# Performance work log

Hardware: AMD Instinct MI355X
Metric: run time of the kernel (lower is better)

## Reference

```python
import jax, jax.numpy as jnp
import numpy as np

B, V, D, R = 2, 4096, 192, 16
E, H = 2 * D, 8
DH = E // H
K, TK = 16, 8


def _ln(x, g, b):
    m = x.mean(-1, keepdims=True)
    v = ((x - m) ** 2).mean(-1, keepdims=True)
    return (x - m) * jax.lax.rsqrt(v + 1e-5) * g + b


def _coords():
    # voxel centers in [-1,1]^3, (V,3)
    r = (jnp.arange(R, dtype=jnp.float32) + 0.5) / R * 2.0 - 1.0
    return jnp.stack(jnp.meshgrid(r, r, r, indexing='ij'), -1).reshape(-1, 3)


def setup_inputs() -> dict:
    key = jax.random.key(0)
    ks = jax.random.split(key, 10)
    s = 0.02
    return {
        'voxel_tokens': jax.random.normal(ks[0], (B, V, D), jnp.float32),
        'non_empty_mask': jax.random.randint(ks[1], (B, V), 0, 2).astype(bool),
        'We': jax.random.normal(ks[2], (D, E)) * s, 'be': jnp.zeros((E,)),
        'g1': jnp.ones((E,)), 'bt1': jnp.zeros((E,)),
        'Wqkv': jax.random.normal(ks[3], (E, 3 * E)) * s, 'bqkv': jnp.zeros((3 * E,)),
        'Wo': jax.random.normal(ks[4], (E, E)) * s, 'bo': jnp.zeros((E,)),
        'Wc': jax.random.normal(ks[5], (E, D)) * s, 'bc': jnp.zeros((D,)),
        'g2': jnp.ones((E,)), 'bt2': jnp.zeros((E,)),
        'W1': jax.random.normal(ks[6], (E, 2 * E)) * s, 'b1': jnp.zeros((2 * E,)),
        'W2': jax.random.normal(ks[7], (2 * E, E)) * s, 'b2': jnp.zeros((E,)),
    }


def reference(voxel_tokens, non_empty_mask, We, be, g1, bt1, Wqkv, bqkv, Wo, bo,
              Wc, bc, g2, bt2, W1, b1, W2, b2):
    fmask = non_empty_mask.astype(voxel_tokens.dtype)  # (B,V)
    shortcut = voxel_tokens
    x = voxel_tokens @ We + be                          # expand: (B,V,E)
    x = _ln(x, g1, bt1)
    # --- sparse dynamic voxel attention ---
    c = _coords()
    d2 = jnp.sum((c[:, None, :] - c[None, :, :]) ** 2, -1)  # (V,V)
    big = jnp.asarray(1e9, x.dtype)
    dmask = d2[None] + (1.0 - fmask)[:, None, :] * big      # empty keys pushed away
    _, knn = jax.lax.top_k(-dmask, K)                        # (B,V,K) nearest non-empty
    qkv = x @ Wqkv + bqkv
    q, k, v = jnp.split(qkv, 3, axis=-1)                     # (B,V,E) each
    bidx = jnp.arange(B)[:, None, None]
    kn = k[bidx, knn].reshape(B, V, K, H, DH)                # gathered neighbor keys
    vn = v[bidx, knn].reshape(B, V, K, H, DH)
    qh = q.reshape(B, V, H, DH)
    scores = jnp.einsum('bvhd,bvkhd->bvhk', qh, kn) / jnp.sqrt(jnp.asarray(DH, x.dtype))
    nvalid = fmask[bidx, knn]                                # (B,V,K)
    scores = jnp.where(nvalid[:, :, None, :] > 0, scores, -big)
    sel, sidx = jax.lax.top_k(scores, TK)                    # top_k_select by score
    attn = jax.nn.softmax(sel, axis=-1)                      # (B,V,H,TK)
    vt = vn.transpose(0, 1, 3, 2, 4)                         # (B,V,H,K,DH)
    vsel = jnp.take_along_axis(vt, sidx[..., None], axis=3)  # (B,V,H,TK,DH)
    o = jnp.einsum('bvhk,bvhkd->bvhd', attn, vsel).reshape(B, V, E)
    o = o @ Wo + bo
    # masked scatter: empty voxels -> zeros (reconstruct_dense_masked_scatter_2)
    x = o * fmask[..., None]
    x = x @ Wc + bc                                          # contract
    x = x * 0.5 + shortcut                                   # DropPath(0) -> identity
    x2 = x @ We + be
    x2 = _ln(x2, g2, bt2)
    x2 = jax.nn.gelu(x2 @ W1 + b1) @ W2 + b2                 # FeedForward(E, 2E)
    x2 = x2 @ Wc + bc
    return x2 * 0.5 + x
```

## Files before the change

kernel.cpp:

```cpp
#include <hip/hip_runtime.h>
#include <stdint.h>


using u16 = unsigned short;
using u32 = unsigned int;
using u64 = unsigned long long;

typedef short short8 __attribute__((ext_vector_type(8)));
typedef float f32x4 __attribute__((ext_vector_type(4)));

#define DEV static __device__ __forceinline__

constexpr int cV = 4096, cD = 192;
constexpr int cE = 384;
constexpr int cKN = 16, cTK = 8;
constexpr int cM = 2 * cV;
constexpr int c3E = 1152;

DEV float bf2f(u16 v) { return __uint_as_float(((u32)v) << 16); }
DEV float bflo(u32 v) { return __uint_as_float(v << 16); }
DEV float bfhi(u32 v) { return __uint_as_float(v & 0xFFFF0000u); }
DEV u16 f2bf(float f) {
  u32 u = __float_as_uint(f);
  u = (u + 0x7FFFu + ((u >> 16) & 1u)) >> 16;
  return (u16)u;
}
DEV int mget(const void* mp, int flag, int i) {
  if (flag == 0) return ((const int*)mp)[i] != 0;
  if (flag == 1) return ((const float*)mp)[i] != 0.0f;
  if (flag == 2) return ((const u16*)mp)[i] != 0;
  return ((const unsigned char*)mp)[i] != 0;
}
DEV float gelu_tanh(float x) {
  float t = tanhf(0.7978845608028654f * (x + 0.044715f * x * x * x));
  return 0.5f * x * (1.0f + t);
}
DEV u32 f2ord(float f) {
  u32 u = __float_as_uint(f);
  return (u & 0x80000000u) ? ~u : (u | 0x80000000u);
}
DEV float ord2f(u32 o) {
  u32 bits = (o & 0x80000000u) ? (o & 0x7FFFFFFFu) : ~o;
  return __uint_as_float(bits);
}
DEV int bf_plausible(u32 h) {
  if (h == 0u || h == 0x8000u) return 1;
  u32 e = (h >> 7) & 0xFFu;
  return (e >= 100u && e <= 140u) ? 1 : 0;
}

using as1p = const unsigned int __attribute__((address_space(1)))*;
using as3p = unsigned int __attribute__((address_space(3)))*;
DEV void gload16(const void* g, void* l) {
  __builtin_amdgcn_global_load_lds((as1p)g, (as3p)l, 16, 0, 0);
}
DEV f32x4 mfma16x16x32_bf16(short8 a, short8 b, f32x4 c) {
  asm volatile("v_mfma_f32_16x16x32_bf16 %0, %1, %2, %0" : "+v"(c) : "v"(a), "v"(b));
  return c;
}
DEV int swz(int row, int byteoff) { return byteoff ^ ((row & 7) << 4); }
DEV int ldswz(int r, int c) { return r * 64 + (c ^ ((r & 7) * 8)); }

#define SBPIN() __builtin_amdgcn_sched_barrier(0)
#define VMW(N) do { \
  __builtin_amdgcn_sched_barrier(0); \
  asm volatile("s_waitcnt vmcnt(" #N ")" ::: "memory"); \
  __builtin_amdgcn_sched_barrier(0); \
} while (0)

template <int T, typename AF>
DEV void stage_1x8(const u16* __restrict__ wbase, int Kst, u16* bpriv,
                   int l15, int l4, int sr, int scs,
                   f32x4 (&acc)[2][3], AF&& aread) {
  #pragma unroll
  for (int i = 0; i < 6; ++i)
    gload16(wbase + (size_t)(i * 8 + sr) * Kst + scs, (char*)bpriv + i * 1024);
  SBPIN();
  #pragma unroll
  for (int t = 0; t < T; ++t) {
    if (t + 1 < T) {
      #pragma unroll
      for (int i = 0; i < 6; ++i)
        gload16(wbase + (size_t)(i * 8 + sr) * Kst + (t + 1) * 64 + scs,
                (char*)bpriv + ((t + 1) & 1) * 6144 + i * 1024);
      VMW(6);
    } else {
      VMW(0);
    }
    const u16* bb = bpriv + (t & 1) * 3072;
    #pragma unroll
    for (int ks = 0; ks < 2; ++ks) {
      short8 a0 = aread(0, t, ks);
      short8 a1 = aread(1, t, ks);
      #pragma unroll
      for (int n = 0; n < 3; ++n) {
        short8 b = *(const short8*)&bb[ldswz(n * 16 + l15, ks * 32 + l4 * 8)];
        acc[0][n] = mfma16x16x32_bf16(a0, b, acc[0][n]);
        acc[1][n] = mfma16x16x32_bf16(a1, b, acc[1][n]);
      }
    }
    SBPIN();
  }
}

template <int T, typename AF>
DEV void stage_2x4(const u16* __restrict__ wbase, int Kst, u16* bpriv,
                   int l15, int l4, int sr, int scs,
                   f32x4 (&acc)[3], AF&& aread) {
  #pragma unroll
  for (int i = 0; i < 6; ++i)
    gload16(wbase + (size_t)(i * 8 + sr) * Kst + scs, (char*)bpriv + i * 1024);
  SBPIN();
  #pragma unroll
  for (int t = 0; t < T; ++t) {
    if (t + 1 < T) {
      #pragma unroll
      for (int i = 0; i < 6; ++i)
        gload16(wbase + (size_t)(i * 8 + sr) * Kst + (t + 1) * 64 + scs,
                (char*)bpriv + ((t + 1) & 1) * 6144 + i * 1024);
      VMW(6);
    } else {
      VMW(0);
    }
    const u16* bb = bpriv + (t & 1) * 3072;
    #pragma unroll
    for (int ks = 0; ks < 2; ++ks) {
      short8 a = aread(t, ks);
      #pragma unroll
      for (int n = 0; n < 3; ++n) {
        short8 b = *(const short8*)&bb[ldswz(n * 16 + l15, ks * 32 + l4 * 8)];
        acc[n] = mfma16x16x32_bf16(a, b, acc[n]);
      }
    }
    SBPIN();
  }
}

__global__ void detect_all_kernel(const u32* __restrict__ tok,
                                  const u32* __restrict__ m,
                                  int* __restrict__ flag) {
  __shared__ int cnt, sa, sb, sc;
  if (threadIdx.x == 0) { cnt = 0; sa = 0; sb = 0; sc = 0; }
  __syncthreads();
  int c = 0;
  for (int i = threadIdx.x; i < 4096; i += 256) {
    u32 d = tok[i];
    c += bf_plausible(d & 0xFFFFu) & bf_plausible(d >> 16);
  }
  atomicAdd(&cnt, c);
  int a = 0, b = 0, cc = 0;
  for (int i = threadIdx.x; i < 2048; i += 256) {
    u32 d = m[i];
    if (!(d == 0u || d == 1u)) a = 1;
    if (!(d == 0u || d == 0x3F800000u)) b = 1;
    if (!(d == 0u || d == 0x00003F80u || d == 0x3F800000u || d == 0x3F803F80u)) cc = 1;
  }
  if (a) atomicOr(&sa, 1);
  if (b) atomicOr(&sb, 1);
  if (cc) atomicOr(&sc, 1);
  __syncthreads();
  if (threadIdx.x == 0) {
    flag[1] = (cnt > 3400) ? 1 : 0;
    flag[0] = (sa == 0) ? 0 : ((sb == 0) ? 1 : ((sc == 0) ? 2 : 3));
  }
}

struct PrepArgs {
  const void* csrc[11]; u16* cdst[11]; int cn[11];
  const void* tsrc[6]; u16* tdst[6]; int tK[6]; int tN[6];
  const void* mask; u64* bm;
};
__global__ __launch_bounds__(256) void prep_kernel(PrepArgs a, const int* __restrict__ flag) {
  const int job = blockIdx.y;
  const int dt = flag[1];
  if (job < 11) {
    const int n = a.cn[job];
    u16* d = a.cdst[job];
    if (dt) {
      const u16* s = (const u16*)a.csrc[job];
      for (int i = blockIdx.x * 256 + threadIdx.x; i < n; i += gridDim.x * 256) d[i] = s[i];
    } else {
      const float* s = (const float*)a.csrc[job];
      for (int i = blockIdx.x * 256 + threadIdx.x; i < n; i += gridDim.x * 256) d[i] = f2bf(s[i]);
    }
  } else if (job < 17) {
    const int t = job - 11;
    const int K = a.tK[t], N = a.tN[t];
    const int total = K * N;
    u16* d = a.tdst[t];
    for (int i = blockIdx.x * 256 + threadIdx.x; i < total; i += gridDim.x * 256) {
      int n = i / K, k = i - n * K;
      u16 vv;
      if (dt) vv = ((const u16*)a.tsrc[t])[(size_t)k * N + n];
      else vv = f2bf(((const float*)a.tsrc[t])[(size_t)k * N + n]);
      d[i] = vv;
    }
  } else {
    const int gw = (blockIdx.x * 256 + threadIdx.x) >> 6;
    const int lane = threadIdx.x & 63;
    if (gw < 128) {
      const int fl = flag[0];
      u64 bal = __ballot(mget(a.mask, fl, gw * 64 + lane) != 0);
      if (lane == 0) a.bm[gw] = bal;
    }
  }
}

__global__ __launch_bounds__(256) void knn_kernel(const u64* __restrict__ bitmask,
                                                  int* __restrict__ knn_out) {
  const int tid = threadIdx.x;
  const int wid = tid >> 6, lane = tid & 63;
  const int q0 = blockIdx.x * 4;
  const int b = q0 >> 12;
  const int q = q0 + wid;
  const int v = q & 4095;
  __shared__ u64 smask[64];
  __shared__ int hist4[4][64];
  __shared__ int listT[4][64];
  __shared__ int out16s[4][16];
  __shared__ int meta[4][3];
  __shared__ int cntA[4], cntT[4];
  if (tid < 64) smask[tid] = bitmask[b * 64 + tid];
  for (int i = tid; i < 4 * 64; i += 256) ((int*)hist4)[i] = 0;
  if (lane == 0) { cntA[wid] = 0; cntT[wid] = 0; }
  __syncthreads();
  const int iv = v >> 8, jv = (v >> 4) & 15, kv = v & 15;
  #pragma unroll
  for (int t = 0; t < 12; ++t) {
    int o = t * 64 + lane;
    if (o < 729) {
      int oi = o / 81, rm = o - oi * 81;
      int oj = rm / 9, ok = rm - oj * 9;
      int i = iv + oi - 4, j = jv + oj - 4, k = kv + ok - 4;
      if (((i | j | k) & ~15) == 0) {
        int u = (i << 8) | (j << 4) | k;
        if ((smask[u >> 6] >> (u & 63)) & 1ull) {
          int di = oi - 4, dj = oj - 4, dk = ok - 4;
          atomicAdd(&hist4[wid][di * di + dj * dj + dk * dk], 1);
        }
      }
    }
  }
  __syncthreads();
  if (lane == 0) {
    int cum = 0, T = -1, below = 0;
    for (int d = 0; d <= 48; ++d) {
      int h = hist4[wid][d];
      if (h > 0 && cum + h >= cKN) { T = d; below = cum; break; }
      cum += h;
    }
    if (T > 24) T = -1;
    meta[wid][0] = T; meta[wid][1] = below; meta[wid][2] = (T < 0) ? 1 : 0;
  }
  __syncthreads();
  const int T = meta[wid][0], below = meta[wid][1], fb = meta[wid][2];
  #pragma unroll
  for (int t = 0; t < 12; ++t) {
    int o = t * 64 + lane;
    if (o < 729) {
      int oi = o / 81, rm = o - oi * 81;
      int oj = rm / 9, ok = rm - oj * 9;
      int i = iv + oi - 4, j = jv + oj - 4, k = kv + ok - 4;
      if (((i | j | k) & ~15) == 0) {
        int u = (i << 8) | (j << 4) | k;
        if ((smask[u >> 6] >> (u & 63)) & 1ull) {
          int di = oi - 4, dj = oj - 4, dk = ok - 4;
          int d2 = di * di + dj * dj + dk * dk;
          if (d2 < T) { int p = atomicAdd(&cntA[wid], 1); out16s[wid][p] = u; }
          else if (d2 == T) { int p = atomicAdd(&cntT[wid], 1); if (p < 64) listT[wid][p] = u; }
        }
      }
    }
  }
  __syncthreads();
  if (!fb) {
    if (lane == 0) {
      int need = cKN - below;
      int nT = cntT[wid] < 64 ? cntT[wid] : 64;
      for (int r = 0; r < need; ++r) {
        int bi = 0, bu = 0x7FFFFFFF;
        for (int i2 = 0; i2 < nT; ++i2) { int x = listT[wid][i2]; if (x < bu) { bu = x; bi = i2; } }
        out16s[wid][below + r] = bu;
        listT[wid][bi] = 0x7FFFFFFF;
      }
    }
  } else {
    u64 rem = smask[lane];
    const int myi = lane >> 2;
    const int di2 = (iv - myi) * (iv - myi);
    for (int r = 0; r < cKN; ++r) {
      u64 tmp = rem;
      u32 best = 0xFFFFFFFFu;
      while (tmp) {
        int bp = __builtin_ctzll(tmp);
        tmp &= tmp - 1;
        int u = (lane << 6) | bp;
        int dj = jv - ((u >> 4) & 15), dk = kv - (u & 15);
        u32 key = (u32)(((di2 + dj * dj + dk * dk) << 12) | u);
        if (key < best) best = key;
      }
      u32 pk = (best == 0xFFFFFFFFu) ? 0xFFFFFFFFu : ((best << 6) | (u32)lane);
      #pragma unroll
      for (int off = 1; off < 64; off <<= 1) {
        u32 o2 = __shfl_xor(pk, off);
        if (o2 < pk) pk = o2;
      }
      int u = (int)((pk >> 6) & 4095u);
      int wl = (int)(pk & 63u);
      if (lane == wl) rem &= ~(1ull << (u & 63));
      if (lane == 0) out16s[wid][r] = u;
    }
  }
  __syncthreads();
  if (lane < cKN) knn_out[q * cKN + lane] = out16s[wid][lane];
}

__global__ __launch_bounds__(512) void fused_ln_qkv(
    const u16* __restrict__ tokc, const u16* __restrict__ WeT,
    const u16* __restrict__ be, const u16* __restrict__ g1, const u16* __restrict__ bt1,
    const u16* __restrict__ WqkvT, const u16* __restrict__ bqkv,
    u16* __restrict__ QB) {
  __shared__ alignas(16) u16 Afull[3 * 2048];
  __shared__ alignas(16) u16 Bst[8][2][3072];
  __shared__ alignas(16) char X1[32 * 768];
  __shared__ float st[32][8][2];
  const int tid = threadIdx.x;
  const int lane = tid & 63, wn = tid >> 6;
  const int l15 = lane & 15, l4 = lane >> 4;
  const int sr = lane >> 3;
  const int scs = (((lane & 7) ^ sr) << 3);
  const int row0 = blockIdx.x * 32;
  u16* bpriv = &Bst[wn][0][0];

  for (int g = wn; g < 12; g += 8)
    gload16(tokc + (size_t)(row0 + (g & 3) * 8 + sr) * 192 + (g >> 2) * 64 + scs,
            (char*)Afull + g * 1024);
  SBPIN();
  __syncthreads();

  f32x4 acc[2][3];
  #pragma unroll
  for (int m = 0; m < 2; ++m)
    #pragma unroll
    for (int n = 0; n < 3; ++n) acc[m][n] = f32x4{0.f, 0.f, 0.f, 0.f};
  stage_1x8<3>(WeT + (size_t)(wn * 48) * 192, 192, bpriv, l15, l4, sr, scs, acc,
               [&](int m, int t, int ks) {
                 return *(const short8*)&Afull[t * 2048 + ldswz(m * 16 + l15, ks * 32 + l4 * 8)];
               });
  float s[2][4], sq[2][4];
  #pragma unroll
  for (int m = 0; m < 2; ++m)
    #pragma unroll
    for (int j = 0; j < 4; ++j) { s[m][j] = 0.f; sq[m][j] = 0.f; }
  #pragma unroll
  for (int n = 0; n < 3; ++n) {
    const float bi = bf2f(be[wn * 48 + n * 16 + l15]);
    #pragma unroll
    for (int m = 0; m < 2; ++m)
      #pragma unroll
      for (int j = 0; j < 4; ++j) {
        acc[m][n][j] += bi;
        s[m][j] += acc[m][n][j]; sq[m][j] += acc[m][n][j] * acc[m][n][j];
      }
  }
  #pragma unroll
  for (int off = 1; off < 16; off <<= 1)
    #pragma unroll
    for (int m = 0; m < 2; ++m)
      #pragma unroll
      for (int j = 0; j < 4; ++j) { s[m][j] += __shfl_xor(s[m][j], off); sq[m][j] += __shfl_xor(sq[m][j], off); }
  if (l15 == 0) {
    #pragma unroll
    for (int m = 0; m < 2; ++m)
      #pragma unroll
      for (int j = 0; j < 4; ++j) {
        const int rl = m * 16 + l4 * 4 + j;
        st[rl][wn][0] = s[m][j]; st[rl][wn][1] = sq[m][j];
      }
  }
  __syncthreads();
  #pragma unroll
  for (int m = 0; m < 2; ++m)
    #pragma unroll
    for (int j = 0; j < 4; ++j) {
      const int rl = m * 16 + l4 * 4 + j;
      float ts = 0.f, tq = 0.f;
      #pragma unroll
      for (int wv = 0; wv < 8; ++wv) { ts += st[rl][wv][0]; tq += st[rl][wv][1]; }
      const float mean = ts * (1.0f / 384.0f);
      const float var = tq * (1.0f / 384.0f) - mean * mean;
      const float rstd = rsqrtf(var + 1e-5f);
      #pragma unroll
      for (int n = 0; n < 3; ++n) {
        const int col = wn * 48 + n * 16 + l15;
        const float v = (acc[m][n][j] - mean) * rstd * bf2f(g1[col]) + bf2f(bt1[col]);
        *(u16*)(X1 + swz(rl, rl * 768 + col * 2)) = f2bf(v);
      }
    }
  __syncthreads();

  for (int chunk = 0; chunk < 3; ++chunk) {
    f32x4 a2[2][3];
    #pragma unroll
    for (int m = 0; m < 2; ++m)
      #pragma unroll
      for (int n = 0; n < 3; ++n) a2[m][n] = f32x4{0.f, 0.f, 0.f, 0.f};
    stage_1x8<6>(WqkvT + (size_t)(chunk * 384 + wn * 48) * 384, 384, bpriv,
                 l15, l4, sr, scs, a2,
                 [&](int m, int t, int ks) {
                   const int rl = m * 16 + l15;
                   return *(const short8*)(X1 + swz(rl, rl * 768 + (t * 64 + ks * 32 + l4 * 8) * 2));
                 });
    #pragma unroll
    for (int n = 0; n < 3; ++n) {
      const int col = chunk * 384 + wn * 48 + n * 16 + l15;
      const float bi = bf2f(bqkv[col]);
      #pragma unroll
      for (int m = 0; m < 2; ++m)
        #pragma unroll
        for (int j = 0; j < 4; ++j)
          QB[(size_t)(row0 + m * 16 + l4 * 4 + j) * c3E + col] = f2bf(a2[m][n][j] + bi);
    }
  }
}

__global__ __launch_bounds__(512) void fused_cd(
    const u16* __restrict__ S2, const u16* __restrict__ WoT, const u16* __restrict__ bo,
    const void* __restrict__ mask, const int* __restrict__ flag,
    const u16* __restrict__ WcT, const u16* __restrict__ bc, const u16* __restrict__ tokc,
    const u16* __restrict__ WeT, const u16* __restrict__ be,
    const u16* __restrict__ g2, const u16* __restrict__ bt2,
    const u16* __restrict__ W1T, const u16* __restrict__ b1,
    const u16* __restrict__ W2T, const u16* __restrict__ b2,
    void* __restrict__ outv) {
  __shared__ alignas(16) u16 Afull[6 * 2048];
  __shared__ alignas(16) u16 Bst[8][2][3072];
  __shared__ alignas(16) char Tb[32 * 768];
  __shared__ float st[32][8][2];
  char* HbA = (char*)Afull;
  const int tid = threadIdx.x;
  const int lane = tid & 63, wn = tid >> 6;
  const int wr = wn >> 2, wc = wn & 3;
  const int l15 = lane & 15, l4 = lane >> 4;
  const int sr = lane >> 3;
  const int scs = (((lane & 7) ^ sr) << 3);
  const int row0 = blockIdx.x * 32;
  const int fl = flag[0];
  u16* bpriv = &Bst[wn][0][0];

  for (int g = wn; g < 24; g += 8)
    gload16(S2 + (size_t)(row0 + (g & 3) * 8 + sr) * cE + (g >> 2) * 64 + scs,
            (char*)Afull + g * 1024);
  SBPIN();
  __syncthreads();

  {
    f32x4 acc[2][3];
    #pragma unroll
    for (int m = 0; m < 2; ++m)
      #pragma unroll
      for (int n = 0; n < 3; ++n) acc[m][n] = f32x4{0.f, 0.f, 0.f, 0.f};
    stage_1x8<6>(WoT + (size_t)(wn * 48) * 384, 384, bpriv, l15, l4, sr, scs, acc,
                 [&](int m, int t, int ks) {
                   return *(const short8*)&Afull[t * 2048 + ldswz(m * 16 + l15, ks * 32 + l4 * 8)];
                 });
    #pragma unroll
    for (int m = 0; m < 2; ++m)
      #pragma unroll
      for (int j = 0; j < 4; ++j) {
        const int rl = m * 16 + l4 * 4 + j;
        const float fm = mget(mask, fl, row0 + rl) ? 1.0f : 0.0f;
        #pragma unroll
        for (int n = 0; n < 3; ++n) {
          const int col = wn * 48 + n * 16 + l15;
          const float v = (acc[m][n][j] + bf2f(bo[col])) * fm;
          *(u16*)(Tb + swz(rl, rl * 768 + col * 2)) = f2bf(v);
        }
      }
  }
  __syncthreads();

  f32x4 xm[3];
  #pragma unroll
  for (int n = 0; n < 3; ++n) xm[n] = f32x4{0.f, 0.f, 0.f, 0.f};
  stage_2x4<6>(WcT + (size_t)(wc * 48) * 384, 384, bpriv, l15, l4, sr, scs, xm,
               [&](int t, int ks) {
                 const int rl = wr * 16 + l15;
                 return *(const short8*)(Tb + swz(rl, rl * 768 + (t * 64 + ks * 32 + l4 * 8) * 2));
               });
  __syncthreads();
  #pragma unroll
  for (int n = 0; n < 3; ++n) {
    const int col = wc * 48 + n * 16 + l15;
    const float bi = bf2f(bc[col]);
    #pragma unroll
    for (int j = 0; j < 4; ++j) {
      const int rl = wr * 16 + l4 * 4 + j;
      xm[n][j] = (xm[n][j] + bi) * 0.5f + bf2f(tokc[(size_t)(row0 + rl) * cD + col]);
      *(u16*)(Tb + swz(rl, rl * 384 + col * 2)) = f2bf(xm[n][j]);
    }
  }
  __syncthreads();

  {
    f32x4 a3[2][3];
    #pragma unroll
    for (int m = 0; m < 2; ++m)
      #pragma unroll
      for (int n = 0; n < 3; ++n) a3[m][n] = f32x4{0.f, 0.f, 0.f, 0.f};
    stage_1x8<3>(WeT + (size_t)(wn * 48) * 192, 192, bpriv, l15, l4, sr, scs, a3,
                 [&](int m, int t, int ks) {
                   const int rl = m * 16 + l15;
                   return *(const short8*)(Tb + swz(rl, rl * 384 + (t * 64 + ks * 32 + l4 * 8) * 2));
                 });
    float s[2][4], sq[2][4];
    #pragma unroll
    for (int m = 0; m < 2; ++m)
      #pragma unroll
      for (int j = 0; j < 4; ++j) { s[m][j] = 0.f; sq[m][j] = 0.f; }
    #pragma unroll
    for (int n = 0; n < 3; ++n) {
      const float bi = bf2f(be[wn * 48 + n * 16 + l15]);
      #pragma unroll
      for (int m = 0; m < 2; ++m)
        #pragma unroll
        for (int j = 0; j < 4; ++j) {
          a3[m][n][j] += bi;
          s[m][j] += a3[m][n][j]; sq[m][j] += a3[m][n][j] * a3[m][n][j];
        }
    }
    #pragma unroll
    for (int off = 1; off < 16; off <<= 1)
      #pragma unroll
      for (int m = 0; m < 2; ++m)
        #pragma unroll
        for (int j = 0; j < 4; ++j) { s[m][j] += __shfl_xor(s[m][j], off); sq[m][j] += __shfl_xor(sq[m][j], off); }
    if (l15 == 0) {
      #pragma unroll
      for (int m = 0; m < 2; ++m)
        #pragma unroll
        for (int j = 0; j < 4; ++j) {
          const int rl = m * 16 + l4 * 4 + j;
          st[rl][wn][0] = s[m][j]; st[rl][wn][1] = sq[m][j];
        }
    }
    __syncthreads();
    #pragma unroll
    for (int m = 0; m < 2; ++m)
      #pragma unroll
      for (int j = 0; j < 4; ++j) {
        const int rl = m * 16 + l4 * 4 + j;
        float ts = 0.f, tq = 0.f;
        #pragma unroll
        for (int wv = 0; wv < 8; ++wv) { ts += st[rl][wv][0]; tq += st[rl][wv][1]; }
        const float mean = ts * (1.0f / 384.0f);
        const float var = tq * (1.0f / 384.0f) - mean * mean;
        const float rstd = rsqrtf(var + 1e-5f);
        #pragma unroll
        for (int n = 0; n < 3; ++n) {
          const int col = wn * 48 + n * 16 + l15;
          const float v = (a3[m][n][j] - mean) * rstd * bf2f(g2[col]) + bf2f(bt2[col]);
          *(u16*)(Tb + swz(rl, rl * 768 + col * 2)) = f2bf(v);
        }
      }
  }
  __syncthreads();

  f32x4 accF[2][3];
  #pragma unroll
  for (int m = 0; m < 2; ++m)
    #pragma unroll
    for (int n = 0; n < 3; ++n) accF[m][n] = f32x4{0.f, 0.f, 0.f, 0.f};

  for (int half = 0; half < 2; ++half) {
    {
      f32x4 a1[2][3];
      #pragma unroll
      for (int m = 0; m < 2; ++m)
        #pragma unroll
        for (int n = 0; n < 3; ++n) a1[m][n] = f32x4{0.f, 0.f, 0.f, 0.f};
      stage_1x8<6>(W1T + (size_t)(half * 384 + wn * 48) * 384, 384, bpriv,
                   l15, l4, sr, scs, a1,
                   [&](int m, int t, int ks) {
                     const int rl = m * 16 + l15;
                     return *(const short8*)(Tb + swz(rl, rl * 768 + (t * 64 + ks * 32 + l4 * 8) * 2));
                   });
      #pragma unroll
      for (int n = 0; n < 3; ++n) {
        const int col = wn * 48 + n * 16 + l15;
        const float bi = bf2f(b1[half * 384 + col]);
        #pragma unroll
        for (int m = 0; m < 2; ++m)
          #pragma unroll
          for (int j = 0; j < 4; ++j) {
            const int rl = m * 16 + l4 * 4 + j;
            *(u16*)(HbA + swz(rl, rl * 768 + col * 2)) = f2bf(gelu_tanh(a1[m][n][j] + bi));
          }
      }
    }
    __syncthreads();
    stage_1x8<6>(W2T + (size_t)(wn * 48) * 768 + half * 384, 768, bpriv,
                 l15, l4, sr, scs, accF,
                 [&](int m, int t, int ks) {
                   const int rl = m * 16 + l15;
                   return *(const short8*)(HbA + swz(rl, rl * 768 + (t * 64 + ks * 32 + l4 * 8) * 2));
                 });
    __syncthreads();
  }
  #pragma unroll
  for (int n = 0; n < 3; ++n) {
    const int col = wn * 48 + n * 16 + l15;
    const float bi = bf2f(b2[col]);
    #pragma unroll
    for (int m = 0; m < 2; ++m)
      #pragma unroll
      for (int j = 0; j < 4; ++j) {
        const int rl = m * 16 + l4 * 4 + j;
        *(u16*)(HbA + swz(rl, rl * 768 + col * 2)) = f2bf(accF[m][n][j] + bi);
      }
  }
  __syncthreads();
  f32x4 a3[3];
  #pragma unroll
  for (int n = 0; n < 3; ++n) a3[n] = f32x4{0.f, 0.f, 0.f, 0.f};
  stage_2x4<6>(WcT + (size_t)(wc * 48) * 384, 384, bpriv, l15, l4, sr, scs, a3,
               [&](int t, int ks) {
                 const int rl = wr * 16 + l15;
                 return *(const short8*)(HbA + swz(rl, rl * 768 + (t * 64 + ks * 32 + l4 * 8) * 2));
               });
  u16* o16 = (u16*)outv;
  float* o32 = (float*)outv;
  const int dtf = flag[1];
  #pragma unroll
  for (int n = 0; n < 3; ++n) {
    const int col = wc * 48 + n * 16 + l15;
    const float bi = bf2f(bc[col]);
    #pragma unroll
    for (int j = 0; j < 4; ++j) {
      const int rl = wr * 16 + l4 * 4 + j;
      const size_t oi = (size_t)(row0 + rl) * cD + col;
      const float r = (a3[n][j] + bi) * 0.5f + xm[n][j];
      if (dtf) o16[oi] = f2bf(r);
      else o32[oi] = r;
    }
  }
}

__global__ __launch_bounds__(256) void attn_kernel(const u16* __restrict__ qkv,
                                                   const int* __restrict__ knn,
                                                   u16* __restrict__ o_out) {
  const int wid = threadIdx.x >> 6;
  const int lane = threadIdx.x & 63;
  const int bq = blockIdx.x * 4 + wid;
  const int b = bq >> 12;
  __shared__ float w4[4][8][8];
  __shared__ int vid4[4][8][8];
  __shared__ int nb4[4][16];
  float (*w)[8] = w4[wid];
  int (*vid)[8] = vid4[wid];
  int* nb = nb4[wid];
  if (lane < 16) nb[lane] = knn[bq * cKN + lane];
  const int h = lane >> 3;
  const int j = lane & 7;
  const uint2* qp = (const uint2*)(qkv + (size_t)bq * c3E + h * 48);
  const int r0 = nb[j], r1 = nb[j + 8];
  const uint2* k0p = (const uint2*)(qkv + ((size_t)(b * cV + r0)) * c3E + cE + h * 48);
  const uint2* k1p = (const uint2*)(qkv + ((size_t)(b * cV + r1)) * c3E + cE + h * 48);
  float s0 = 0.f, s1 = 0.f;
  #pragma unroll
  for (int t = 0; t < 12; ++t) {
    uint2 qv = qp[t];
    uint2 k0 = k0p[t];
    uint2 k1 = k1p[t];
    s0 += bflo(qv.x) * bflo(k0.x) + bfhi(qv.x) * bfhi(k0.x)
        + bflo(qv.y) * bflo(k0.y) + bfhi(qv.y) * bfhi(k0.y);
    s1 += bflo(qv.x) * bflo(k1.x) + bfhi(qv.x) * bfhi(k1.x)
        + bflo(qv.y) * bflo(k1.y) + bfhi(qv.y) * bfhi(k1.y);
  }
  const float inv = 0.14433756729740643f;
  u64 key0 = (((u64)f2ord(s0 * inv)) << 4) | (u64)(15 - j);
  u64 key1 = (((u64)f2ord(s1 * inv)) << 4) | (u64)(15 - (j + 8));
  float m0 = 0.f, Z = 0.f, myw = 0.f;
  int myv = 0;
  #pragma unroll
  for (int r = 0; r < cTK; ++r) {
    u64 best = key0 > key1 ? key0 : key1;
    u64 o1 = __shfl_xor(best, 1); if (o1 > best) best = o1;
    u64 o2 = __shfl_xor(best, 2); if (o2 > best) best = o2;
    u64 o4 = __shfl_xor(best, 4); if (o4 > best) best = o4;
    if (key0 == best) key0 = 0;
    if (key1 == best) key1 = 0;
    float sv = ord2f((u32)(best >> 4));
    int nsel = 15 - (int)(best & 15ull);
    if (r == 0) m0 = sv;
    float e = expf(sv - m0);
    Z += e;
    if (j == r) { myw = e; myv = nsel; }
  }
  w[h][j] = myw / Z;
  vid[h][j] = nb[myv];
  const u16* vbase = qkv + (size_t)(b * cV) * c3E + 2 * cE;
  #pragma unroll
  for (int rep = 0; rep < 6; ++rep) {
    int e = rep * 64 + lane;
    int h2 = e / 48;
    float acc = 0.f;
    #pragma unroll
    for (int t = 0; t < cTK; ++t)
      acc += w[h2][t] * bf2f(vbase[(size_t)vid[h2][t] * c3E + e]);
    o_out[(size_t)bq * cE + e] = f2bf(acc);
  }
}

extern "C" void kernel_launch(void* const* d_in, const int* in_sizes, int n_in,
                              void* d_out, int out_size, void* d_ws, size_t ws_size,
                              hipStream_t stream) {
  if (n_in < 18) return;
  const void* mask = d_in[1];

  char* ws = (char*)d_ws;
  size_t off = 0;
  auto alloc = [&](size_t bytes) { size_t o = off; off += (bytes + 255) & ~(size_t)255; return o; };
  int* flag  = (int*)(ws + alloc(256));
  u64* bmask = (u64*)(ws + alloc(128 * 8));
  int* knn   = (int*)(ws + alloc((size_t)cM * cKN * 4));
  u16* S2    = (u16*)(ws + alloc((size_t)cM * cE * 2));
  u16* QB    = (u16*)(ws + alloc((size_t)cM * c3E * 2));
  u16* tokc  = (u16*)(ws + alloc((size_t)cM * cD * 2));
  u16* be    = (u16*)(ws + alloc(cE * 2));
  u16* g1    = (u16*)(ws + alloc(cE * 2));
  u16* bt1   = (u16*)(ws + alloc(cE * 2));
  u16* bqkv  = (u16*)(ws + alloc(c3E * 2));
  u16* bo    = (u16*)(ws + alloc(cE * 2));
  u16* bc    = (u16*)(ws + alloc(cD * 2));
  u16* g2    = (u16*)(ws + alloc(cE * 2));
  u16* bt2   = (u16*)(ws + alloc(cE * 2));
  u16* b1    = (u16*)(ws + alloc(2 * cE * 2));
  u16* b2    = (u16*)(ws + alloc(cE * 2));
  u16* WeT   = (u16*)(ws + alloc((size_t)384 * 192 * 2));
  u16* WqkvT = (u16*)(ws + alloc((size_t)1152 * 384 * 2));
  u16* WoT   = (u16*)(ws + alloc((size_t)384 * 384 * 2));
  u16* WcT   = (u16*)(ws + alloc((size_t)256 * 384 * 2));
  u16* W1T   = (u16*)(ws + alloc((size_t)768 * 384 * 2));
  u16* W2T   = (u16*)(ws + alloc((size_t)384 * 768 * 2));
  (void)ws_size; (void)in_sizes; (void)out_size;

  detect_all_kernel<<<1, 256, 0, stream>>>((const u32*)d_in[0], (const u32*)mask, flag);

  {
    PrepArgs pa;
    const int csrci[11] = {0, 3, 4, 5, 7, 9, 11, 12, 13, 15, 17};
    u16* cdsts[11] = {tokc, be, g1, bt1, bqkv, bo, bc, g2, bt2, b1, b2};
    const int cns[11] = {cM * cD, cE, cE, cE, c3E, cE, cD, cE, cE, 2 * cE, cE};
    for (int i = 0; i < 11; ++i) { pa.csrc[i] = d_in[csrci[i]]; pa.cdst[i] = cdsts[i]; pa.cn[i] = cns[i]; }
    const int tsrci[6] = {2, 6, 8, 10, 14, 16};
    u16* tdsts[6] = {WeT, WqkvT, WoT, WcT, W1T, W2T};
    const int tKs[6] = {192, 384, 384, 384, 384, 768};
    const int tNs[6] = {384, 1152, 384, 192, 768, 384};
    for (int i = 0; i < 6; ++i) { pa.tsrc[i] = d_in[tsrci[i]]; pa.tdst[i] = tdsts[i]; pa.tK[i] = tKs[i]; pa.tN[i] = tNs[i]; }
    pa.mask = mask; pa.bm = bmask;
    prep_kernel<<<dim3(96, 18), 256, 0, stream>>>(pa, flag);
  }

  knn_kernel<<<cM / 4, 256, 0, stream>>>(bmask, knn);

  const int GB = cM / 32;
  fused_ln_qkv<<<GB, 512, 0, stream>>>(tokc, WeT, be, g1, bt1, WqkvT, bqkv, QB);
  attn_kernel<<<cM / 4, 256, 0, stream>>>(QB, knn, S2);
  fused_cd<<<GB, 512, 0, stream>>>(S2, WoT, bo, mask, flag, WcT, bc, tokc,
                                   WeT, be, g2, bt2, W1T, b1, W2T, b2, d_out);
}
```

Measured before the change: 150.9 us.

## Pre-swizzle weights into MFMA fragment order and load B operands straight into registers

The prep kernel now writes each weight matrix in a per-lane MFMA B-fragment layout (16 columns by 32 k per 512-element block). The GEMM stages then read B fragments straight from global memory into registers with double-buffered register prefetch, instead of staging them through per-wave LDS buffers with global_load_lds and explicit vmcnt waits. This drops the 96KB per-block Bst LDS allocation, which can raise occupancy, and removes the LDS read traffic for B. In exchange it uses more registers for the prefetch buffers and relies on the compiler to place waits, since the explicit scheduling barriers are gone.

```diff
diff --git a/kernel.cpp b/kernel.cpp
--- a/kernel.cpp
+++ b/kernel.cpp
@@ -60,79 +60,55 @@
 }
 DEV int swz(int row, int byteoff) { return byteoff ^ ((row & 7) << 4); }
 DEV int ldswz(int r, int c) { return r * 64 + (c ^ ((r & 7) * 8)); }
-
 #define SBPIN() __builtin_amdgcn_sched_barrier(0)
-#define VMW(N) do { \
-  __builtin_amdgcn_sched_barrier(0); \
-  asm volatile("s_waitcnt vmcnt(" #N ")" ::: "memory"); \
-  __builtin_amdgcn_sched_barrier(0); \
-} while (0)
+
+struct BF { short8 v[3][2]; };
+DEV void loadBF(BF& b, const u16* __restrict__ fbase, int nKB, int kb, int lane) {
+  #pragma unroll
+  for (int n = 0; n < 3; ++n)
+    #pragma unroll
+    for (int ks = 0; ks < 2; ++ks)
+      b.v[n][ks] = *(const short8*)(fbase + ((size_t)n * nKB + kb + ks) * 512 + lane * 8);
+}
 
 template <int T, typename AF>
-DEV void stage_1x8(const u16* __restrict__ wbase, int Kst, u16* bpriv,
-                   int l15, int l4, int sr, int scs,
-                   f32x4 (&acc)[2][3], AF&& aread) {
-  #pragma unroll
-  for (int i = 0; i < 6; ++i)
-    gload16(wbase + (size_t)(i * 8 + sr) * Kst + scs, (char*)bpriv + i * 1024);
-  SBPIN();
+DEV void rstage_1x8(const u16* __restrict__ fbase, int nKB, int kb0,
+                    int lane, int l15, int l4,
+                    f32x4 (&acc)[2][3], AF&& aread) {
+  BF bp[2];
+  loadBF(bp[0], fbase, nKB, kb0, lane);
   #pragma unroll
   for (int t = 0; t < T; ++t) {
-    if (t + 1 < T) {
-      #pragma unroll
-      for (int i = 0; i < 6; ++i)
-        gload16(wbase + (size_t)(i * 8 + sr) * Kst + (t + 1) * 64 + scs,
-                (char*)bpriv + ((t + 1) & 1) * 6144 + i * 1024);
-      VMW(6);
-    } else {
-      VMW(0);
-    }
-    const u16* bb = bpriv + (t & 1) * 3072;
+    if (t + 1 < T) loadBF(bp[(t + 1) & 1], fbase, nKB, kb0 + 2 * (t + 1), lane);
     #pragma unroll
     for (int ks = 0; ks < 2; ++ks) {
       short8 a0 = aread(0, t, ks);
       short8 a1 = aread(1, t, ks);
       #pragma unroll
       for (int n = 0; n < 3; ++n) {
-        short8 b = *(const short8*)&bb[ldswz(n * 16 + l15, ks * 32 + l4 * 8)];
-        acc[0][n] = mfma16x16x32_bf16(a0, b, acc[0][n]);
-        acc[1][n] = mfma16x16x32_bf16(a1, b, acc[1][n]);
-      }
-    }
-    SBPIN();
+        acc[0][n] = mfma16x16x32_bf16(a0, bp[t & 1].v[n][ks], acc[0][n]);
+        acc[1][n] = mfma16x16x32_bf16(a1, bp[t & 1].v[n][ks], acc[1][n]);
+      }
+    }
   }
 }
 
 template <int T, typename AF>
-DEV void stage_2x4(const u16* __restrict__ wbase, int Kst, u16* bpriv,
-                   int l15, int l4, int sr, int scs,
-                   f32x4 (&acc)[3], AF&& aread) {
-  #pragma unroll
-  for (int i = 0; i < 6; ++i)
-    gload16(wbase + (size_t)(i * 8 + sr) * Kst + scs, (char*)bpriv + i * 1024);
-  SBPIN();
+DEV void rstage_2x4(const u16* __restrict__ fbase, int nKB, int kb0,
+                    int lane, int l15, int l4,
+                    f32x4 (&acc)[3], AF&& aread) {
+  BF bp[2];
+  loadBF(bp[0], fbase, nKB, kb0, lane);
   #pragma unroll
   for (int t = 0; t < T; ++t) {
-    if (t + 1 < T) {
-      #pragma unroll
-      for (int i = 0; i < 6; ++i)
-        gload16(wbase + (size_t)(i * 8 + sr) * Kst + (t + 1) * 64 + scs,
-                (char*)bpriv + ((t + 1) & 1) * 6144 + i * 1024);
-      VMW(6);
-    } else {
-      VMW(0);
-    }
-    const u16* bb = bpriv + (t & 1) * 3072;
+    if (t + 1 < T) loadBF(bp[(t + 1) & 1], fbase, nKB, kb0 + 2 * (t + 1), lane);
     #pragma unroll
     for (int ks = 0; ks < 2; ++ks) {
       short8 a = aread(t, ks);
       #pragma unroll
-      for (int n = 0; n < 3; ++n) {
-        short8 b = *(const short8*)&bb[ldswz(n * 16 + l15, ks * 32 + l4 * 8)];
-        acc[n] = mfma16x16x32_bf16(a, b, acc[n]);
-      }
-    }
-    SBPIN();
+      for (int n = 0; n < 3; ++n)
+        acc[n] = mfma16x16x32_bf16(a, bp[t & 1].v[n][ks], acc[n]);
+    }
   }
 }
 
@@ -186,10 +162,18 @@
   } else if (job < 17) {
     const int t = job - 11;
     const int K = a.tK[t], N = a.tN[t];
+    const int nKB = K >> 5;
     const int total = K * N;
     u16* d = a.tdst[t];
     for (int i = blockIdx.x * 256 + threadIdx.x; i < total; i += gridDim.x * 256) {
-      int n = i / K, k = i - n * K;
+      const int frag = i >> 9;
+      const int r = i & 511;
+      const int lane = r >> 3, e = r & 7;
+      const int l4 = lane >> 4, l15 = lane & 15;
+      const int colblk = frag / nKB;
+      const int kblk = frag - colblk * nKB;
+      const int n = colblk * 16 + l15;
+      const int k = kblk * 32 + l4 * 8 + e;
       u16 vv;
       if (dt) vv = ((const u16*)a.tsrc[t])[(size_t)k * N + n];
       else vv = f2bf(((const float*)a.tsrc[t])[(size_t)k * N + n]);
@@ -316,12 +300,11 @@
 }
 
 __global__ __launch_bounds__(512) void fused_ln_qkv(
-    const u16* __restrict__ tokc, const u16* __restrict__ WeT,
+    const u16* __restrict__ tokc, const u16* __restrict__ WeF,
     const u16* __restrict__ be, const u16* __restrict__ g1, const u16* __restrict__ bt1,
-    const u16* __restrict__ WqkvT, const u16* __restrict__ bqkv,
+    const u16* __restrict__ WqkvF, const u16* __restrict__ bqkv,
     u16* __restrict__ QB) {
   __shared__ alignas(16) u16 Afull[3 * 2048];
-  __shared__ alignas(16) u16 Bst[8][2][3072];
   __shared__ alignas(16) char X1[32 * 768];
   __shared__ float st[32][8][2];
   const int tid = threadIdx.x;
@@ -330,7 +313,6 @@
   const int sr = lane >> 3;
   const int scs = (((lane & 7) ^ sr) << 3);
   const int row0 = blockIdx.x * 32;
-  u16* bpriv = &Bst[wn][0][0];
 
   for (int g = wn; g < 12; g += 8)
     gload16(tokc + (size_t)(row0 + (g & 3) * 8 + sr) * 192 + (g >> 2) * 64 + scs,
@@ -343,10 +325,10 @@
   for (int m = 0; m < 2; ++m)
     #pragma unroll
     for (int n = 0; n < 3; ++n) acc[m][n] = f32x4{0.f, 0.f, 0.f, 0.f};
-  stage_1x8<3>(WeT + (size_t)(wn * 48) * 192, 192, bpriv, l15, l4, sr, scs, acc,
-               [&](int m, int t, int ks) {
-                 return *(const short8*)&Afull[t * 2048 + ldswz(m * 16 + l15, ks * 32 + l4 * 8)];
-               });
+  rstage_1x8<3>(WeF + (size_t)(wn * 3) * 6 * 512, 6, 0, lane, l15, l4, acc,
+                [&](int m, int t, int ks) {
+                  return *(const short8*)&Afull[t * 2048 + ldswz(m * 16 + l15, ks * 32 + l4 * 8)];
+                });
   float s[2][4], sq[2][4];
   #pragma unroll
   for (int m = 0; m < 2; ++m)
@@ -405,12 +387,11 @@
     for (int m = 0; m < 2; ++m)
       #pragma unroll
       for (int n = 0; n < 3; ++n) a2[m][n] = f32x4{0.f, 0.f, 0.f, 0.f};
-    stage_1x8<6>(WqkvT + (size_t)(chunk * 384 + wn * 48) * 384, 384, bpriv,
-                 l15, l4, sr, scs, a2,
-                 [&](int m, int t, int ks) {
-                   const int rl = m * 16 + l15;
-                   return *(const short8*)(X1 + swz(rl, rl * 768 + (t * 64 + ks * 32 + l4 * 8) * 2));
-                 });
+    rstage_1x8<6>(WqkvF + (size_t)(chunk * 24 + wn * 3) * 12 * 512, 12, 0, lane, l15, l4, a2,
+                  [&](int m, int t, int ks) {
+                    const int rl = m * 16 + l15;
+                    return *(const short8*)(X1 + swz(rl, rl * 768 + (t * 64 + ks * 32 + l4 * 8) * 2));
+                  });
     #pragma unroll
     for (int n = 0; n < 3; ++n) {
       const int col = chunk * 384 + wn * 48 + n * 16 + l15;
@@ -425,16 +406,15 @@
 }
 
 __global__ __launch_bounds__(512) void fused_cd(
-    const u16* __restrict__ S2, const u16* __restrict__ WoT, const u16* __restrict__ bo,
+    const u16* __restrict__ S2, const u16* __restrict__ WoF, const u16* __restrict__ bo,
     const void* __restrict__ mask, const int* __restrict__ flag,
-    const u16* __restrict__ WcT, const u16* __restrict__ bc, const u16* __restrict__ tokc,
-    const u16* __restrict__ WeT, const u16* __restrict__ be,
+    const u16* __restrict__ WcF, const u16* __restrict__ bc, const u16* __restrict__ tokc,
+    const u16* __restrict__ WeF, const u16* __restrict__ be,
     const u16* __restrict__ g2, const u16* __restrict__ bt2,
-    const u16* __restrict__ W1T, const u16* __restrict__ b1,
-    const u16* __restrict__ W2T, const u16* __restrict__ b2,
+    const u16* __restrict__ W1F, const u16* __restrict__ b1,
+    const u16* __restrict__ W2F, const u16* __restrict__ b2,
     void* __restrict__ outv) {
   __shared__ alignas(16) u16 Afull[6 * 2048];
-  __shared__ alignas(16) u16 Bst[8][2][3072];
   __shared__ alignas(16) char Tb[32 * 768];
   __shared__ float st[32][8][2];
   char* HbA = (char*)Afull;
@@ -446,7 +426,6 @@
   const int scs = (((lane & 7) ^ sr) << 3);
   const int row0 = blockIdx.x * 32;
   const int fl = flag[0];
-  u16* bpriv = &Bst[wn][0][0];
 
   for (int g = wn; g < 24; g += 8)
     gload16(S2 + (size_t)(row0 + (g & 3) * 8 + sr) * cE + (g >> 2) * 64 + scs,
@@ -460,10 +439,10 @@
     for (int m = 0; m < 2; ++m)
       #pragma unroll
       for (int n = 0; n < 3; ++n) acc[m][n] = f32x4{0.f, 0.f, 0.f, 0.f};
-    stage_1x8<6>(WoT + (size_t)(wn * 48) * 384, 384, bpriv, l15, l4, sr, scs, acc,
-                 [&](int m, int t, int ks) {
-                   return *(const short8*)&Afull[t * 2048 + ldswz(m * 16 + l15, ks * 32 + l4 * 8)];
-                 });
+    rstage_1x8<6>(WoF + (size_t)(wn * 3) * 12 * 512, 12, 0, lane, l15, l4, acc,
+                  [&](int m, int t, int ks) {
+                    return *(const short8*)&Afull[t * 2048 + ldswz(m * 16 + l15, ks * 32 + l4 * 8)];
+                  });
     #pragma unroll
     for (int m = 0; m < 2; ++m)
       #pragma unroll
@@ -483,11 +462,11 @@
   f32x4 xm[3];
   #pragma unroll
   for (int n = 0; n < 3; ++n) xm[n] = f32x4{0.f, 0.f, 0.f, 0.f};
-  stage_2x4<6>(WcT + (size_t)(wc * 48) * 384, 384, bpriv, l15, l4, sr, scs, xm,
-               [&](int t, int ks) {
-                 const int rl = wr * 16 + l15;
-                 return *(const short8*)(Tb + swz(rl, rl * 768 + (t * 64 + ks * 32 + l4 * 8) * 2));
-               });
+  rstage_2x4<6>(WcF + (size_t)(wc * 3) * 12 * 512, 12, 0, lane, l15, l4, xm,
+                [&](int t, int ks) {
+                  const int rl = wr * 16 + l15;
+                  return *(const short8*)(Tb + swz(rl, rl * 768 + (t * 64 + ks * 32 + l4 * 8) * 2));
+                });
   __syncthreads();
   #pragma unroll
   for (int n = 0; n < 3; ++n) {
@@ -508,11 +487,11 @@
     for (int m = 0; m < 2; ++m)
       #pragma unroll
       for (int n = 0; n < 3; ++n) a3[m][n] = f32x4{0.f, 0.f, 0.f, 0.f};
-    stage_1x8<3>(WeT + (size_t)(wn * 48) * 192, 192, bpriv, l15, l4, sr, scs, a3,
-                 [&](int m, int t, int ks) {
-                   const int rl = m * 16 + l15;
-                   return *(const short8*)(Tb + swz(rl, rl * 384 + (t * 64 + ks * 32 + l4 * 8) * 2));
-                 });
+    rstage_1x8<3>(WeF + (size_t)(wn * 3) * 6 * 512, 6, 0, lane, l15, l4, a3,
+                  [&](int m, int t, int ks) {
+                    const int rl = m * 16 + l15;
+                    return *(const short8*)(Tb + swz(rl, rl * 384 + (t * 64 + ks * 32 + l4 * 8) * 2));
+                  });
     float s[2][4], sq[2][4];
     #pragma unroll
     for (int m = 0; m < 2; ++m)
@@ -579,12 +558,11 @@
       for (int m = 0; m < 2; ++m)
         #pragma unroll
         for (int n = 0; n < 3; ++n) a1[m][n] = f32x4{0.f, 0.f, 0.f, 0.f};
-      stage_1x8<6>(W1T + (size_t)(half * 384 + wn * 48) * 384, 384, bpriv,
-                   l15, l4, sr, scs, a1,
-                   [&](int m, int t, int ks) {
-                     const int rl = m * 16 + l15;
-                     return *(const short8*)(Tb + swz(rl, rl * 768 + (t * 64 + ks * 32 + l4 * 8) * 2));
-                   });
+      rstage_1x8<6>(W1F + (size_t)(half * 24 + wn * 3) * 12 * 512, 12, 0, lane, l15, l4, a1,
+                    [&](int m, int t, int ks) {
+                      const int rl = m * 16 + l15;
+                      return *(const short8*)(Tb + swz(rl, rl * 768 + (t * 64 + ks * 32 + l4 * 8) * 2));
+                    });
       #pragma unroll
       for (int n = 0; n < 3; ++n) {
         const int col = wn * 48 + n * 16 + l15;
@@ -599,12 +577,11 @@
       }
     }
     __syncthreads();
-    stage_1x8<6>(W2T + (size_t)(wn * 48) * 768 + half * 384, 768, bpriv,
-                 l15, l4, sr, scs, accF,
-                 [&](int m, int t, int ks) {
-                   const int rl = m * 16 + l15;
-                   return *(const short8*)(HbA + swz(rl, rl * 768 + (t * 64 + ks * 32 + l4 * 8) * 2));
-                 });
+    rstage_1x8<6>(W2F + (size_t)(wn * 3) * 24 * 512, 24, half * 12, lane, l15, l4, accF,
+                  [&](int m, int t, int ks) {
+                    const int rl = m * 16 + l15;
+                    return *(const short8*)(HbA + swz(rl, rl * 768 + (t * 64 + ks * 32 + l4 * 8) * 2));
+                  });
     __syncthreads();
   }
   #pragma unroll
@@ -623,11 +600,11 @@
   f32x4 a3[3];
   #pragma unroll
   for (int n = 0; n < 3; ++n) a3[n] = f32x4{0.f, 0.f, 0.f, 0.f};
-  stage_2x4<6>(WcT + (size_t)(wc * 48) * 384, 384, bpriv, l15, l4, sr, scs, a3,
-               [&](int t, int ks) {
-                 const int rl = wr * 16 + l15;
-                 return *(const short8*)(HbA + swz(rl, rl * 768 + (t * 64 + ks * 32 + l4 * 8) * 2));
-               });
+  rstage_2x4<6>(WcF + (size_t)(wc * 3) * 12 * 512, 12, 0, lane, l15, l4, a3,
+                [&](int t, int ks) {
+                  const int rl = wr * 16 + l15;
+                  return *(const short8*)(HbA + swz(rl, rl * 768 + (t * 64 + ks * 32 + l4 * 8) * 2));
+                });
   u16* o16 = (u16*)outv;
   float* o32 = (float*)outv;
   const int dtf = flag[1];
@@ -737,12 +714,12 @@
   u16* bt2   = (u16*)(ws + alloc(cE * 2));
   u16* b1    = (u16*)(ws + alloc(2 * cE * 2));
   u16* b2    = (u16*)(ws + alloc(cE * 2));
-  u16* WeT   = (u16*)(ws + alloc((size_t)384 * 192 * 2));
-  u16* WqkvT = (u16*)(ws + alloc((size_t)1152 * 384 * 2));
-  u16* WoT   = (u16*)(ws + alloc((size_t)384 * 384 * 2));
-  u16* WcT   = (u16*)(ws + alloc((size_t)256 * 384 * 2));
-  u16* W1T   = (u16*)(ws + alloc((size_t)768 * 384 * 2));
-  u16* W2T   = (u16*)(ws + alloc((size_t)384 * 768 * 2));
+  u16* WeF   = (u16*)(ws + alloc((size_t)192 * 384 * 2));
+  u16* WqkvF = (u16*)(ws + alloc((size_t)384 * 1152 * 2));
+  u16* WoF   = (u16*)(ws + alloc((size_t)384 * 384 * 2));
+  u16* WcF   = (u16*)(ws + alloc((size_t)384 * 192 * 2));
+  u16* W1F   = (u16*)(ws + alloc((size_t)384 * 768 * 2));
+  u16* W2F   = (u16*)(ws + alloc((size_t)768 * 384 * 2));
   (void)ws_size; (void)in_sizes; (void)out_size;
 
   detect_all_kernel<<<1, 256, 0, stream>>>((const u32*)d_in[0], (const u32*)mask, flag);
@@ -754,7 +731,7 @@
     const int cns[11] = {cM * cD, cE, cE, cE, c3E, cE, cD, cE, cE, 2 * cE, cE};
     for (int i = 0; i < 11; ++i) { pa.csrc[i] = d_in[csrci[i]]; pa.cdst[i] = cdsts[i]; pa.cn[i] = cns[i]; }
     const int tsrci[6] = {2, 6, 8, 10, 14, 16};
-    u16* tdsts[6] = {WeT, WqkvT, WoT, WcT, W1T, W2T};
+    u16* tdsts[6] = {WeF, WqkvF, WoF, WcF, W1F, W2F};
     const int tKs[6] = {192, 384, 384, 384, 384, 768};
     const int tNs[6] = {384, 1152, 384, 192, 768, 384};
     for (int i = 0; i < 6; ++i) { pa.tsrc[i] = d_in[tsrci[i]]; pa.tdst[i] = tdsts[i]; pa.tK[i] = tKs[i]; pa.tN[i] = tNs[i]; }
@@ -765,8 +742,8 @@
   knn_kernel<<<cM / 4, 256, 0, stream>>>(bmask, knn);
 
   const int GB = cM / 32;
-  fused_ln_qkv<<<GB, 512, 0, stream>>>(tokc, WeT, be, g1, bt1, WqkvT, bqkv, QB);
+  fused_ln_qkv<<<GB, 512, 0, stream>>>(tokc, WeF, be, g1, bt1, WqkvF, bqkv, QB);
   attn_kernel<<<cM / 4, 256, 0, stream>>>(QB, knn, S2);
-  fused_cd<<<GB, 512, 0, stream>>>(S2, WoT, bo, mask, flag, WcT, bc, tokc,
-                                   WeT, be, g2, bt2, W1T, b1, W2T, b2, d_out);
-}
+  fused_cd<<<GB, 512, 0, stream>>>(S2, WoF, bo, mask, flag, WcF, bc, tokc,
+                                   WeF, be, g2, bt2, W1F, b1, W2F, b2, d_out);
+}
```

Result: faster. 140.7 us (median of 2 runs) (-6.8%).
